# Kernel tuning notes

Hardware: AMD Instinct MI355X
Metric: run time of the kernel (lower is better)

The kernel has to match this reference:

```python
import jax, jax.numpy as jnp
import numpy as np

N, E, H, L = 50000, 400000, 100, 2
NF, EF = 16, 8
BN_EPS = 1e-5  # torch BatchNorm1d eps; eval mode with running_mean=0, running_var=1


def setup_inputs() -> dict:
    key = jax.random.key(0)
    ks = jax.random.split(key, 32)
    s = 0.05
    rn = lambda k, shape: jax.random.normal(k, shape, dtype=jnp.float32) * s
    return {
        "x": jax.random.normal(ks[0], (N, NF), dtype=jnp.float32),
        "edge_index": jax.random.randint(ks[1], (2, E), 0, N, dtype=jnp.int32),
        "edge_attr": jax.random.normal(ks[2], (E, EF), dtype=jnp.float32),
        "node_w": rn(ks[3], (NF, H)), "node_b": rn(ks[4], (H,)),
        "edge_w": rn(ks[5], (EF, H)), "edge_b": rn(ks[6], (H,)),
        "conv_w1": rn(ks[7], (L, H, H)), "conv_b1": rn(ks[8], (L, H)),
        "conv_w2": rn(ks[9], (L, H, H)), "conv_b2": rn(ks[10], (L, H)),
        "bn_gamma": jnp.ones((L, H), jnp.float32), "bn_beta": jnp.zeros((L, H), jnp.float32),
        "em_w1": rn(ks[11], (L, 3 * H, H)), "em_b1": rn(ks[12], (L, H)),
        "em_w2": rn(ks[13], (L, H, H)), "em_b2": rn(ks[14], (L, H)),
        "mlp_w1": rn(ks[15], (3 * H, 50)), "mlp_b1": rn(ks[16], (50,)),
        "mlp_w2": rn(ks[17], (50, 25)), "mlp_b2": rn(ks[18], (25,)),
        "mlp_w3": rn(ks[19], (25, 1)), "mlp_b3": rn(ks[20], (1,)),
    }


def reference(x, edge_index, edge_attr, node_w, node_b, edge_w, edge_b,
              conv_w1, conv_b1, conv_w2, conv_b2, bn_gamma, bn_beta,
              em_w1, em_b1, em_w2, em_b2,
              mlp_w1, mlp_b1, mlp_w2, mlp_b2, mlp_w3, mlp_b3):
    src, dst = edge_index[0], edge_index[1]
    h = x @ node_w + node_b            # [N,H]
    e = edge_attr @ edge_w + edge_b    # [E,H]
    bn_inv = 1.0 / jnp.sqrt(1.0 + BN_EPS)
    for i in range(L):
        # GINEConv (eps=0): MLP(x + sum_{j->i} relu(x_j + e_ji))
        msg = jax.nn.relu(h[src] + e)                                  # [E,H]
        agg = jax.ops.segment_sum(msg, dst, num_segments=h.shape[0])   # [N,H]
        z = h + agg
        z = jax.nn.relu(z @ conv_w1[i] + conv_b1[i]) @ conv_w2[i] + conv_b2[i]
        bn = z * (bn_gamma[i] * bn_inv) + bn_beta[i]                   # BN eval (mean 0, var 1)
        h = (h + jax.nn.relu(bn)) * 0.5
        ei = jnp.concatenate([h[src], h[dst], e], axis=-1)             # [E,3H]
        e = e + (jax.nn.relu(ei @ em_w1[i] + em_b1[i]) @ em_w2[i] + em_b2[i]) * 0.5
    xe = jnp.concatenate([h[src], h[dst], e], axis=-1)                 # [E,3H]
    o = jax.nn.relu(xe @ mlp_w1 + mlp_b1)
    o = jax.nn.relu(o @ mlp_w2 + mlp_b2)
    return (o @ mlp_w3 + mlp_b3)[:, 0]                                 # [E]
```

## Files before the change

### kernel.cpp

```cpp
#include <hip/hip_runtime.h>

#define HD 100
#define NF 16
#define EF 8
#define NN 50000
#define NE 400000
#define NT64 6250

typedef __attribute__((ext_vector_type(8))) short bf16x8;
typedef __attribute__((ext_vector_type(4))) float f32x4;

__device__ __forceinline__ float frelu(float v) { return v > 0.f ? v : 0.f; }
__device__ __forceinline__ unsigned short f2bf(float f) {
  unsigned int u = __float_as_uint(f);
  unsigned int r = (u + 0x7FFF + ((u >> 16) & 1)) >> 16;
  return (unsigned short)r;
}
__device__ __forceinline__ int SWZ(int row, int byte) { return byte ^ ((row & 7) << 4); }
__device__ __forceinline__ float4 L4(const float* p) { return *(const float4*)p; }
__device__ __forceinline__ uint2 pk4(float4 f) {
  uint2 o;
  o.x = (unsigned)f2bf(f.x) | ((unsigned)f2bf(f.y) << 16);
  o.y = (unsigned)f2bf(f.z) | ((unsigned)f2bf(f.w) << 16);
  return o;
}

__device__ __forceinline__ void pack_one(const float* __restrict__ W,
    unsigned short* __restrict__ out, int K, int N, int NT, int t) {
  int lane = t & 63, nt = (t >> 6) % NT, ks = (t >> 6) / NT;
  int kb = ks * 32 + (lane >> 4) * 8, n = nt * 16 + (lane & 15);
  unsigned short v[8];
  #pragma unroll
  for (int j = 0; j < 8; ++j) {
    int k = kb + j;
    float f = (k < K && n < N) ? W[(size_t)k * N + n] : 0.f;
    v[j] = f2bf(f);
  }
  uint4 o4;
  o4.x = (unsigned)v[0] | ((unsigned)v[1] << 16);
  o4.y = (unsigned)v[2] | ((unsigned)v[3] << 16);
  o4.z = (unsigned)v[4] | ((unsigned)v[5] << 16);
  o4.w = (unsigned)v[6] | ((unsigned)v[7] << 16);
  *(uint4*)&out[(size_t)t * 8] = o4;
}

__global__ __launch_bounds__(256) void k_pack_all(
    const float* __restrict__ em_w1, const float* __restrict__ em_w2,
    const float* __restrict__ mlp_w1,
    unsigned short* __restrict__ w1p0, unsigned short* __restrict__ w1p1,
    unsigned short* __restrict__ w2p0, unsigned short* __restrict__ w2p1,
    unsigned short* __restrict__ wf1p) {
  int t = blockIdx.x * 256 + threadIdx.x;
  if (t < 4480)        pack_one(em_w1,          w1p0, 300, 100, 7, t);
  else if (t < 8960)   pack_one(em_w1 + 30000,  w1p1, 300, 100, 7, t - 4480);
  else if (t < 10752)  pack_one(em_w2,          w2p0, 100, 100, 7, t - 8960);
  else if (t < 12544)  pack_one(em_w2 + 10000,  w2p1, 100, 100, 7, t - 10752);
  else if (t < 15104)  pack_one(mlp_w1,         wf1p, 300, 50, 4, t - 12544);
}

__global__ __launch_bounds__(256) void k_node_embed(const float* __restrict__ x,
    const float* __restrict__ w, const float* __restrict__ b, float* __restrict__ h) {
  int t = blockIdx.x * 256 + threadIdx.x;
  int n = t / HD, o = t % HD;
  if (n >= NN) return;
  float acc = b[o];
  #pragma unroll
  for (int k = 0; k < NF; ++k) acc = fmaf(x[n * NF + k], w[k * HD + o], acc);
  h[(size_t)n * HD + o] = acc;
}

__global__ __launch_bounds__(256) void k_edge_embed_perm(const float* __restrict__ ea,
    const int* __restrict__ eids, const float* __restrict__ w, const float* __restrict__ b,
    float* __restrict__ e) {
  __shared__ float ws_[EF * HD];
  __shared__ float bs_[HD];
  int tid = threadIdx.x;
  for (int i = tid; i < EF * HD; i += 256) ws_[i] = w[i];
  for (int i = tid; i < HD; i += 256) bs_[i] = b[i];
  __syncthreads();
  long long t = (long long)blockIdx.x * 256 + tid;
  int p = (int)(t / 25), c4 = (int)(t % 25);
  if (p >= NE) return;
  int eid = eids[p];
  const float* ap = ea + (size_t)eid * EF;
  float4 a0 = L4(ap), a1 = L4(ap + 4);
  float av[8] = {a0.x, a0.y, a0.z, a0.w, a1.x, a1.y, a1.z, a1.w};
  int c0 = c4 * 4;
  float o0 = bs_[c0], o1 = bs_[c0 + 1], o2 = bs_[c0 + 2], o3 = bs_[c0 + 3];
  #pragma unroll
  for (int k = 0; k < EF; ++k) {
    const float* wr = &ws_[k * HD + c0];
    o0 = fmaf(av[k], wr[0], o0); o1 = fmaf(av[k], wr[1], o1);
    o2 = fmaf(av[k], wr[2], o2); o3 = fmaf(av[k], wr[3], o3);
  }
  float4 o; o.x = o0; o.y = o1; o.z = o2; o.w = o3;
  ((float4*)e)[(size_t)p * 25 + c4] = o;
}

__global__ __launch_bounds__(256) void k_hist(const int* __restrict__ dst, int* __restrict__ deg) {
  int eid = blockIdx.x * 256 + threadIdx.x;
  if (eid < NE) atomicAdd(&deg[dst[eid]], 1);
}
__global__ __launch_bounds__(256) void k_scan_part(const int* __restrict__ deg, int* __restrict__ part) {
  __shared__ int sm[256];
  int i = blockIdx.x * 256 + threadIdx.x;
  sm[threadIdx.x] = (i < NN) ? deg[i] : 0;
  __syncthreads();
  for (int s = 128; s > 0; s >>= 1) {
    if (threadIdx.x < s) sm[threadIdx.x] += sm[threadIdx.x + s];
    __syncthreads();
  }
  if (threadIdx.x == 0) part[blockIdx.x] = sm[0];
}
__global__ __launch_bounds__(256) void k_scan_top(int* __restrict__ part, int nb) {
  __shared__ int sm[256];
  int v = (threadIdx.x < nb) ? part[threadIdx.x] : 0;
  sm[threadIdx.x] = v;
  __syncthreads();
  for (int off = 1; off < 256; off <<= 1) {
    int t = (threadIdx.x >= (unsigned)off) ? sm[threadIdx.x - off] : 0;
    __syncthreads();
    sm[threadIdx.x] += t;
    __syncthreads();
  }
  if (threadIdx.x < nb) part[threadIdx.x] = sm[threadIdx.x] - v;
}
__global__ __launch_bounds__(256) void k_scan_fill(const int* __restrict__ deg,
    const int* __restrict__ part, int* __restrict__ rowptr, int* __restrict__ cursor) {
  __shared__ int sm[256];
  int i = blockIdx.x * 256 + threadIdx.x;
  int v = (i < NN) ? deg[i] : 0;
  sm[threadIdx.x] = v;
  __syncthreads();
  for (int off = 1; off < 256; off <<= 1) {
    int t = (threadIdx.x >= (unsigned)off) ? sm[threadIdx.x - off] : 0;
    __syncthreads();
    sm[threadIdx.x] += t;
    __syncthreads();
  }
  int pfx = part[blockIdx.x] + sm[threadIdx.x] - v;
  if (i <= NN) rowptr[i] = pfx;
  if (i < NN) cursor[i] = pfx;
}
__global__ __launch_bounds__(256) void k_fill(const int* __restrict__ dst,
    int* __restrict__ cursor, int* __restrict__ eids) {
  int eid = blockIdx.x * 256 + threadIdx.x;
  if (eid >= NE) return;
  int pos = atomicAdd(&cursor[dst[eid]], 1);
  eids[pos] = eid;
}

__global__ __launch_bounds__(256) void k_gather_node(
    float* __restrict__ h, const float* __restrict__ e,
    const int* __restrict__ rowptr, const int* __restrict__ eids,
    const int* __restrict__ src,
    const float* __restrict__ w1, const float* __restrict__ b1,
    const float* __restrict__ w2, const float* __restrict__ b2,
    const float* __restrict__ gamma, const float* __restrict__ beta) {
  __shared__ float zs[64 * 101];
  int tid = threadIdx.x;
  int base = blockIdx.x * 64;
  {
    int slot = tid >> 2, sub = tid & 3;
    int n = base + slot;
    int cn = n < NN ? n : NN - 1;
    int r0 = rowptr[cn], r1 = rowptr[cn + 1];
    float4 acc[7];
    #pragma unroll
    for (int i = 0; i < 7; ++i) { acc[i].x = 0.f; acc[i].y = 0.f; acc[i].z = 0.f; acc[i].w = 0.f; }
    for (int p = r0; p < r1; ++p) {
      int s = src[eids[p]];
      const float4* hp = (const float4*)&h[(size_t)s * HD];
      const float4* ep = (const float4*)&e[(size_t)p * HD];
      #pragma unroll
      for (int i = 0; i < 7; ++i) {
        int c = sub + i * 4;
        if (c < 25) {
          float4 hv = hp[c], ev = ep[c];
          acc[i].x += frelu(hv.x + ev.x);
          acc[i].y += frelu(hv.y + ev.y);
          acc[i].z += frelu(hv.z + ev.z);
          acc[i].w += frelu(hv.w + ev.w);
        }
      }
    }
    const float4* hn = (const float4*)&h[(size_t)cn * HD];
    #pragma unroll
    for (int i = 0; i < 7; ++i) {
      int c = sub + i * 4;
      if (c < 25) {
        float4 hv = hn[c];
        float* zp = &zs[slot * 101 + c * 4];
        zp[0] = hv.x + acc[i].x;
        zp[1] = hv.y + acc[i].y;
        zp[2] = hv.z + acc[i].z;
        zp[3] = hv.w + acc[i].w;
      }
    }
  }
  __syncthreads();
  int el = tid & 63;
  int o0 = __builtin_amdgcn_readfirstlane((tid >> 6) * 25);
  float* row = &zs[el * 101];
  float acc[25];
  #pragma unroll
  for (int j = 0; j < 25; ++j) acc[j] = b1[o0 + j];
  for (int k = 0; k < HD; ++k) {
    float a = row[k];
    const float* wr = &w1[k * HD + o0];
    #pragma unroll
    for (int j = 0; j < 25; ++j) acc[j] = fmaf(a, wr[j], acc[j]);
  }
  __syncthreads();
  #pragma unroll
  for (int j = 0; j < 25; ++j) row[o0 + j] = frelu(acc[j]);
  __syncthreads();
  float acc2[25];
  #pragma unroll
  for (int j = 0; j < 25; ++j) acc2[j] = b2[o0 + j];
  for (int k = 0; k < HD; ++k) {
    float a = row[k];
    const float* wr = &w2[k * HD + o0];
    #pragma unroll
    for (int j = 0; j < 25; ++j) acc2[j] = fmaf(a, wr[j], acc2[j]);
  }
  int gn = base + el;
  if (gn < NN) {
    const float bninv = 0.99999500003749973f;
    #pragma unroll
    for (int j = 0; j < 25; ++j) {
      int o = o0 + j;
      float bn = acc2[j] * (gamma[o] * bninv) + beta[o];
      h[(size_t)gn * HD + o] = (h[(size_t)gn * HD + o] + frelu(bn)) * 0.5f;
    }
  }
}

__global__ __launch_bounds__(512) void k_edge_mfma(
    const float* __restrict__ h, float* __restrict__ e,
    const int* __restrict__ eids, const int* __restrict__ src, const int* __restrict__ dst,
    const unsigned short* __restrict__ w1p, const float* __restrict__ b1,
    const unsigned short* __restrict__ w2p, const float* __restrict__ b2) {
  __shared__ __align__(16) char lds[151040];
  char* W1L = lds;
  char* W2L = lds + 64512;
  char* A1  = lds + 93184;
  char* A2  = lds + 134144;
  int* ss  = (int*)(lds + 150528);
  int* ds_ = (int*)(lds + 150784);
  int tid = threadIdx.x;
  for (int i = tid; i < 4032; i += 512) ((uint4*)W1L)[i] = ((const uint4*)w1p)[i];
  for (int i = tid; i < 1792; i += 512) ((uint4*)W2L)[i] = ((const uint4*)w2p)[i];

  int lane = tid & 63, w = tid >> 6;
  int l15 = lane & 15, lq = lane >> 4;
  int g = w >> 2;
  int arow = (w & 3) * 16 + l15;
  int ntb = g * 4, ntc = g ? 3 : 4;
  f32x4 zero = {0.f, 0.f, 0.f, 0.f};

  for (int tile = blockIdx.x; tile < NT64; tile += gridDim.x) {
    int base = tile * 64;
    if (tid < 64) { int eid = eids[base + tid]; ss[tid] = src[eid]; ds_[tid] = dst[eid]; }
    __syncthreads();
    for (int idx = tid; idx < 64 * 25; idx += 512) {
      int row = idx / 25, c4 = idx % 25;
      float4 f = ((const float4*)e)[(size_t)(base + row) * 25 + c4];
      *(uint2*)(A1 + SWZ(row, row * 640 + 400 + c4 * 8)) = pk4(f);
    }
    for (int idx = tid; idx < 64 * 25; idx += 512) {
      int row = idx / 25, c4 = idx % 25;
      float4 f = ((const float4*)h)[(size_t)ss[row] * 25 + c4];
      *(uint2*)(A1 + SWZ(row, row * 640 + c4 * 8)) = pk4(f);
    }
    for (int idx = tid; idx < 64 * 25; idx += 512) {
      int row = idx / 25, c4 = idx % 25;
      float4 f = ((const float4*)h)[(size_t)ds_[row] * 25 + c4];
      *(uint2*)(A1 + SWZ(row, row * 640 + 200 + c4 * 8)) = pk4(f);
    }
    for (int idx = tid; idx < 64 * 5; idx += 512) {
      int row = idx / 5, j = idx % 5;
      uint2 z; z.x = 0u; z.y = 0u;
      *(uint2*)(A1 + SWZ(row, row * 640 + 600 + j * 8)) = z;
    }
    __syncthreads();
    f32x4 acc[4];
    #pragma unroll
    for (int i = 0; i < 4; ++i) acc[i] = zero;
    #pragma unroll
    for (int ks = 0; ks < 10; ++ks) {
      bf16x8 a = *(const bf16x8*)(A1 + SWZ(arow, arow * 640 + (ks * 32 + lq * 8) * 2));
      #pragma unroll
      for (int i = 0; i < 4; ++i) {
        if (i < ntc) {
          int nt = ntb + i;
          bf16x8 b = (ks < 9)
            ? *(const bf16x8*)(W1L + ks * 7168 + (nt * 64 + lane) * 16)
            : *(const bf16x8*)(w1p + (size_t)9 * 3584 + (nt * 64 + lane) * 8);
          acc[i] = __builtin_amdgcn_mfma_f32_16x16x32_bf16(a, b, acc[i], 0, 0, 0);
        }
      }
    }
    #pragma unroll
    for (int i = 0; i < 4; ++i) {
      if (i < ntc) {
        int o = (ntb + i) * 16 + l15;
        float bias = (o < HD) ? b1[o] : 0.f;
        #pragma unroll
        for (int ii = 0; ii < 4; ++ii) {
          int r = (w & 3) * 16 + lq * 4 + ii;
          float v = acc[i][ii] + bias;
          v = (o < HD) ? frelu(v) : 0.f;
          *(unsigned short*)(A2 + SWZ(r, r * 256 + o * 2)) = f2bf(v);
        }
      }
    }
    for (int idx = tid; idx < 64 * 8; idx += 512) {
      int r = idx / 8, c = idx % 8;
      *(unsigned int*)(A2 + SWZ(r, r * 256 + 224 + c * 4)) = 0;
    }
    __syncthreads();
    f32x4 acc2[4];
    #pragma unroll
    for (int i = 0; i < 4; ++i) acc2[i] = zero;
    #pragma unroll
    for (int ks = 0; ks < 4; ++ks) {
      bf16x8 a = *(const bf16x8*)(A2 + SWZ(arow, arow * 256 + (ks * 32 + lq * 8) * 2));
      #pragma unroll
      for (int i = 0; i < 4; ++i) {
        if (i < ntc) {
          int nt = ntb + i;
          bf16x8 b = *(const bf16x8*)(W2L + ks * 7168 + (nt * 64 + lane) * 16);
          acc2[i] = __builtin_amdgcn_mfma_f32_16x16x32_bf16(a, b, acc2[i], 0, 0, 0);
        }
      }
    }
    #pragma unroll
    for (int i = 0; i < 4; ++i) {
      if (i < ntc) {
        int o = (ntb + i) * 16 + l15;
        if (o < HD) {
          float bias = b2[o];
          #pragma unroll
          for (int ii = 0; ii < 4; ++ii) {
            int r = (w & 3) * 16 + lq * 4 + ii;
            size_t pp = (size_t)(base + r) * HD + o;
            e[pp] = e[pp] + 0.5f * (acc2[i][ii] + bias);
          }
        }
      }
    }
    __syncthreads();
  }
}

__global__ __launch_bounds__(512) void k_edge_final_mfma(
    const float* __restrict__ h, const float* __restrict__ e,
    const int* __restrict__ eids, const int* __restrict__ src, const int* __restrict__ dst,
    const unsigned short* __restrict__ w1p, const float* __restrict__ b1,
    const unsigned short* __restrict__ w2p, const float* __restrict__ b2,
    const unsigned short* __restrict__ wf1p, const float* __restrict__ fb1,
    const float* __restrict__ fw2, const float* __restrict__ fb2,
    const float* __restrict__ fw3, const float* __restrict__ fb3,
    float* __restrict__ out) {
  __shared__ __align__(16) char lds[156500];
  char* W1L = lds;
  char* W2L = lds + 64512;
  char* A1  = lds + 93184;
  char* A2  = lds + 134144;
  float* W2s = (float*)(lds + 150528);
  float* b2s = (float*)(lds + 155528);
  float* W3s = (float*)(lds + 155628);
  float* b3s = (float*)(lds + 155728);
  int* es  = (int*)(lds + 155732);
  int* ss  = (int*)(lds + 155988);
  int* ds_ = (int*)(lds + 156244);
  int tid = threadIdx.x;
  for (int i = tid; i < 4032; i += 512) ((uint4*)W1L)[i] = ((const uint4*)w1p)[i];
  for (int i = tid; i < 1792; i += 512) ((uint4*)W2L)[i] = ((const uint4*)w2p)[i];
  for (int i = tid; i < 1250; i += 512) W2s[i] = fw2[i];
  if (tid < 25) { b2s[tid] = fb2[tid]; W3s[tid] = fw3[tid]; }
  if (tid == 0) b3s[0] = fb3[0];

  int lane = tid & 63, w = tid >> 6;
  int l15 = lane & 15, lq = lane >> 4;
  int g = w >> 2;
  int arow = (w & 3) * 16 + l15;
  int ntb = g * 4, ntc = g ? 3 : 4;
  f32x4 zero = {0.f, 0.f, 0.f, 0.f};

  for (int tile = blockIdx.x; tile < NT64; tile += gridDim.x) {
    int base = tile * 64;
    if (tid < 64) {
      int eid = eids[base + tid];
      es[tid] = eid; ss[tid] = src[eid]; ds_[tid] = dst[eid];
    }
    __syncthreads();
    for (int idx = tid; idx < 64 * 25; idx += 512) {
      int row = idx / 25, c4 = idx % 25;
      float4 f = ((const float4*)e)[(size_t)(base + row) * 25 + c4];
      *(uint2*)(A1 + SWZ(row, row * 640 + 400 + c4 * 8)) = pk4(f);
    }
    for (int idx = tid; idx < 64 * 25; idx += 512) {
      int row = idx / 25, c4 = idx % 25;
      float4 f = ((const float4*)h)[(size_t)ss[row] * 25 + c4];
      *(uint2*)(A1 + SWZ(row, row * 640 + c4 * 8)) = pk4(f);
    }
    for (int idx = tid; idx < 64 * 25; idx += 512) {
      int row = idx / 25, c4 = idx % 25;
      float4 f = ((const float4*)h)[(size_t)ds_[row] * 25 + c4];
      *(uint2*)(A1 + SWZ(row, row * 640 + 200 + c4 * 8)) = pk4(f);
    }
    for (int idx = tid; idx < 64 * 5; idx += 512) {
      int row = idx / 5, j = idx % 5;
      uint2 z; z.x = 0u; z.y = 0u;
      *(uint2*)(A1 + SWZ(row, row * 640 + 600 + j * 8)) = z;
    }
    __syncthreads();
    f32x4 acc[4];
    #pragma unroll
    for (int i = 0; i < 4; ++i) acc[i] = zero;
    #pragma unroll
    for (int ks = 0; ks < 10; ++ks) {
      bf16x8 a = *(const bf16x8*)(A1 + SWZ(arow, arow * 640 + (ks * 32 + lq * 8) * 2));
      #pragma unroll
      for (int i = 0; i < 4; ++i) {
        if (i < ntc) {
          int nt = ntb + i;
          bf16x8 b = (ks < 9)
            ? *(const bf16x8*)(W1L + ks * 7168 + (nt * 64 + lane) * 16)
            : *(const bf16x8*)(w1p + (size_t)9 * 3584 + (nt * 64 + lane) * 8);
          acc[i] = __builtin_amdgcn_mfma_f32_16x16x32_bf16(a, b, acc[i], 0, 0, 0);
        }
      }
    }
    #pragma unroll
    for (int i = 0; i < 4; ++i) {
      if (i < ntc) {
        int o = (ntb + i) * 16 + l15;
        float bias = (o < HD) ? b1[o] : 0.f;
        #pragma unroll
        for (int ii = 0; ii < 4; ++ii) {
          int r = (w & 3) * 16 + lq * 4 + ii;
          float v = acc[i][ii] + bias;
          v = (o < HD) ? frelu(v) : 0.f;
          *(unsigned short*)(A2 + SWZ(r, r * 256 + o * 2)) = f2bf(v);
        }
      }
    }
    for (int idx = tid; idx < 64 * 8; idx += 512) {
      int r = idx / 8, c = idx % 8;
      *(unsigned int*)(A2 + SWZ(r, r * 256 + 224 + c * 4)) = 0;
    }
    __syncthreads();
    f32x4 acc2[4];
    #pragma unroll
    for (int i = 0; i < 4; ++i) acc2[i] = zero;
    #pragma unroll
    for (int ks = 0; ks < 4; ++ks) {
      bf16x8 a = *(const bf16x8*)(A2 + SWZ(arow, arow * 256 + (ks * 32 + lq * 8) * 2));
      #pragma unroll
      for (int i = 0; i < 4; ++i) {
        if (i < ntc) {
          int nt = ntb + i;
          bf16x8 b = *(const bf16x8*)(W2L + ks * 7168 + (nt * 64 + lane) * 16);
          acc2[i] = __builtin_amdgcn_mfma_f32_16x16x32_bf16(a, b, acc2[i], 0, 0, 0);
        }
      }
    }
    #pragma unroll
    for (int i = 0; i < 4; ++i) {
      if (i < ntc) {
        int o = (ntb + i) * 16 + l15;
        if (o < HD) {
          float bias = b2[o];
          #pragma unroll
          for (int ii = 0; ii < 4; ++ii) {
            int r = (w & 3) * 16 + lq * 4 + ii;
            float ne = e[(size_t)(base + r) * HD + o] + 0.5f * (acc2[i][ii] + bias);
            *(unsigned short*)(A1 + SWZ(r, r * 640 + (200 + o) * 2)) = f2bf(ne);
          }
        }
      }
    }
    __syncthreads();
    f32x4 acc3[2];
    acc3[0] = zero; acc3[1] = zero;
    #pragma unroll
    for (int ks = 0; ks < 10; ++ks) {
      bf16x8 a = *(const bf16x8*)(A1 + SWZ(arow, arow * 640 + (ks * 32 + lq * 8) * 2));
      #pragma unroll
      for (int i = 0; i < 2; ++i) {
        int nt = g * 2 + i;
        bf16x8 b = *(const bf16x8*)(wf1p + ((size_t)(ks * 4 + nt) * 64 + lane) * 8);
        acc3[i] = __builtin_amdgcn_mfma_f32_16x16x32_bf16(a, b, acc3[i], 0, 0, 0);
      }
    }
    __syncthreads();
    #pragma unroll
    for (int i = 0; i < 2; ++i) {
      int o = (g * 2 + i) * 16 + l15;
      if (o < 50) {
        float bias = fb1[o];
        #pragma unroll
        for (int ii = 0; ii < 4; ++ii) {
          int r = (w & 3) * 16 + lq * 4 + ii;
          *(float*)(A2 + r * 208 + o * 4) = frelu(acc3[i][ii] + bias);
        }
      }
    }
    __syncthreads();
    {
      int elg = tid >> 3, q8 = tid & 7;
      const float* trow = (const float*)(A2 + elg * 208);
      float s[4];
      {
        int i = 0;
        #pragma unroll
        for (int j0 = 0; j0 < 25; j0 += 8) { if (j0 + q8 < 25) s[i++] = b2s[j0 + q8]; }
      }
      for (int k = 0; k < 50; ++k) {
        float tv = trow[k];
        int i = 0;
        #pragma unroll
        for (int j0 = 0; j0 < 25; j0 += 8) {
          if (j0 + q8 < 25) { s[i] = fmaf(tv, W2s[k * 25 + j0 + q8], s[i]); ++i; }
        }
      }
      float racc = 0.f;
      {
        int i = 0;
        #pragma unroll
        for (int j0 = 0; j0 < 25; j0 += 8) {
          if (j0 + q8 < 25) { racc = fmaf(frelu(s[i]), W3s[j0 + q8], racc); ++i; }
        }
      }
      racc += __shfl_xor(racc, 1, 8);
      racc += __shfl_xor(racc, 2, 8);
      racc += __shfl_xor(racc, 4, 8);
      if (q8 == 0) out[es[elg]] = racc + b3s[0];
    }
    __syncthreads();
  }
}

extern "C" void kernel_launch(void* const* d_in, const int* in_sizes, int n_in,
                              void* d_out, int out_size, void* d_ws, size_t ws_size,
                              hipStream_t stream) {
  (void)in_sizes; (void)n_in; (void)out_size; (void)ws_size;
  const float* x       = (const float*)d_in[0];
  const int*   eidx    = (const int*)  d_in[1];
  const float* eattr   = (const float*)d_in[2];
  const float* node_w  = (const float*)d_in[3];
  const float* node_b  = (const float*)d_in[4];
  const float* edge_w  = (const float*)d_in[5];
  const float* edge_b  = (const float*)d_in[6];
  const float* conv_w1 = (const float*)d_in[7];
  const float* conv_b1 = (const float*)d_in[8];
  const float* conv_w2 = (const float*)d_in[9];
  const float* conv_b2 = (const float*)d_in[10];
  const float* bn_g    = (const float*)d_in[11];
  const float* bn_b    = (const float*)d_in[12];
  const float* em_w1   = (const float*)d_in[13];
  const float* em_b1   = (const float*)d_in[14];
  const float* em_w2   = (const float*)d_in[15];
  const float* em_b2   = (const float*)d_in[16];
  const float* mlp_w1  = (const float*)d_in[17];
  const float* mlp_b1  = (const float*)d_in[18];
  const float* mlp_w2  = (const float*)d_in[19];
  const float* mlp_b2  = (const float*)d_in[20];
  const float* mlp_w3  = (const float*)d_in[21];
  const float* mlp_b3  = (const float*)d_in[22];

  const int* src = eidx;
  const int* dst = eidx + NE;

  char* ws = (char*)d_ws;
  float* h    = (float*)(ws);
  float* e    = (float*)(ws + 40000000);
  unsigned short* w1p0 = (unsigned short*)(ws + 200000000);
  unsigned short* w1p1 = (unsigned short*)(ws + 200071680);
  unsigned short* w2p0 = (unsigned short*)(ws + 200143360);
  unsigned short* w2p1 = (unsigned short*)(ws + 200172032);
  unsigned short* wf1p = (unsigned short*)(ws + 200200704);
  int* rowptr = (int*)(ws + 200241664);
  int* cursor = (int*)(ws + 200442112);
  int* eids   = (int*)(ws + 200642112);
  int* part   = (int*)(ws + 202242112);

  const int SCAN_NB = (NN + 256) / 256;
  hipMemsetAsync(cursor, 0, (size_t)NN * 4, stream);
  k_hist<<<(NE + 255) / 256, 256, 0, stream>>>(dst, cursor);
  k_scan_part<<<SCAN_NB, 256, 0, stream>>>(cursor, part);
  k_scan_top<<<1, 256, 0, stream>>>(part, SCAN_NB);
  k_scan_fill<<<SCAN_NB, 256, 0, stream>>>(cursor, part, rowptr, cursor);
  k_fill<<<(NE + 255) / 256, 256, 0, stream>>>(dst, cursor, eids);

  k_pack_all<<<(15104 + 255) / 256, 256, 0, stream>>>(
      em_w1, em_w2, mlp_w1, w1p0, w1p1, w2p0, w2p1, wf1p);

  k_node_embed<<<(NN * HD + 255) / 256, 256, 0, stream>>>(x, node_w, node_b, h);
  {
    long long th = (long long)NE * 25;
    k_edge_embed_perm<<<(unsigned)((th + 255) / 256), 256, 0, stream>>>(eattr, eids, edge_w, edge_b, e);
  }

  for (int i = 0; i < 2; ++i) {
    k_gather_node<<<(NN + 63) / 64, 256, 0, stream>>>(
        h, e, rowptr, eids, src,
        conv_w1 + i * HD * HD, conv_b1 + i * HD,
        conv_w2 + i * HD * HD, conv_b2 + i * HD, bn_g + i * HD, bn_b + i * HD);
    if (i == 0) {
      k_edge_mfma<<<256, 512, 0, stream>>>(
          h, e, eids, src, dst, w1p0, em_b1, w2p0, em_b2);
    } else {
      k_edge_final_mfma<<<256, 512, 0, stream>>>(
          h, e, eids, src, dst, w1p1, em_b1 + HD, w2p1, em_b2 + HD,
          wf1p, mlp_b1, mlp_w2, mlp_b2, mlp_w3, mlp_b3, (float*)d_out);
    }
  }
}
```

Before: 835.6 us.

## Double edge-MLP block size to 1024 threads and split N-tiles across more waves

The two edge-MLP MFMA kernels now launch 16 waves per block instead of 8. Each wave group owns two output N-tiles instead of four, and in the final kernel one tile for the first MLP layer. The extra waves are meant to hide LDS and gather latency, since LDS use (about 150 KB) already limits each CU to one block. The tail scalar MLP stage runs on only half the threads, and the larger block may raise register pressure under the 1024-thread launch bound.

```diff
diff --git a/kernel.cpp b/kernel.cpp
--- a/kernel.cpp
+++ b/kernel.cpp
@@ -236,7 +236,7 @@
   }
 }
 
-__global__ __launch_bounds__(512) void k_edge_mfma(
+__global__ __launch_bounds__(1024) void k_edge_mfma(
     const float* __restrict__ h, float* __restrict__ e,
     const int* __restrict__ eids, const int* __restrict__ src, const int* __restrict__ dst,
     const unsigned short* __restrict__ w1p, const float* __restrict__ b1,
@@ -249,49 +249,48 @@
   int* ss  = (int*)(lds + 150528);
   int* ds_ = (int*)(lds + 150784);
   int tid = threadIdx.x;
-  for (int i = tid; i < 4032; i += 512) ((uint4*)W1L)[i] = ((const uint4*)w1p)[i];
-  for (int i = tid; i < 1792; i += 512) ((uint4*)W2L)[i] = ((const uint4*)w2p)[i];
+  for (int i = tid; i < 4032; i += 1024) ((uint4*)W1L)[i] = ((const uint4*)w1p)[i];
+  for (int i = tid; i < 1792; i += 1024) ((uint4*)W2L)[i] = ((const uint4*)w2p)[i];
 
   int lane = tid & 63, w = tid >> 6;
   int l15 = lane & 15, lq = lane >> 4;
   int g = w >> 2;
   int arow = (w & 3) * 16 + l15;
-  int ntb = g * 4, ntc = g ? 3 : 4;
+  int ntb = g * 2, ntc = (g == 3) ? 1 : 2;
   f32x4 zero = {0.f, 0.f, 0.f, 0.f};
 
   for (int tile = blockIdx.x; tile < NT64; tile += gridDim.x) {
     int base = tile * 64;
     if (tid < 64) { int eid = eids[base + tid]; ss[tid] = src[eid]; ds_[tid] = dst[eid]; }
     __syncthreads();
-    for (int idx = tid; idx < 64 * 25; idx += 512) {
+    for (int idx = tid; idx < 64 * 25; idx += 1024) {
       int row = idx / 25, c4 = idx % 25;
       float4 f = ((const float4*)e)[(size_t)(base + row) * 25 + c4];
       *(uint2*)(A1 + SWZ(row, row * 640 + 400 + c4 * 8)) = pk4(f);
     }
-    for (int idx = tid; idx < 64 * 25; idx += 512) {
+    for (int idx = tid; idx < 64 * 25; idx += 1024) {
       int row = idx / 25, c4 = idx % 25;
       float4 f = ((const float4*)h)[(size_t)ss[row] * 25 + c4];
       *(uint2*)(A1 + SWZ(row, row * 640 + c4 * 8)) = pk4(f);
     }
-    for (int idx = tid; idx < 64 * 25; idx += 512) {
+    for (int idx = tid; idx < 64 * 25; idx += 1024) {
       int row = idx / 25, c4 = idx % 25;
       float4 f = ((const float4*)h)[(size_t)ds_[row] * 25 + c4];
       *(uint2*)(A1 + SWZ(row, row * 640 + 200 + c4 * 8)) = pk4(f);
     }
-    for (int idx = tid; idx < 64 * 5; idx += 512) {
-      int row = idx / 5, j = idx % 5;
+    if (tid < 320) {
+      int row = tid / 5, j = tid % 5;
       uint2 z; z.x = 0u; z.y = 0u;
       *(uint2*)(A1 + SWZ(row, row * 640 + 600 + j * 8)) = z;
     }
     __syncthreads();
-    f32x4 acc[4];
-    #pragma unroll
-    for (int i = 0; i < 4; ++i) acc[i] = zero;
+    f32x4 acc[2];
+    acc[0] = zero; acc[1] = zero;
     #pragma unroll
     for (int ks = 0; ks < 10; ++ks) {
       bf16x8 a = *(const bf16x8*)(A1 + SWZ(arow, arow * 640 + (ks * 32 + lq * 8) * 2));
       #pragma unroll
-      for (int i = 0; i < 4; ++i) {
+      for (int i = 0; i < 2; ++i) {
         if (i < ntc) {
           int nt = ntb + i;
           bf16x8 b = (ks < 9)
@@ -302,7 +301,7 @@
       }
     }
     #pragma unroll
-    for (int i = 0; i < 4; ++i) {
+    for (int i = 0; i < 2; ++i) {
       if (i < ntc) {
         int o = (ntb + i) * 16 + l15;
         float bias = (o < HD) ? b1[o] : 0.f;
@@ -315,19 +314,18 @@
         }
       }
     }
-    for (int idx = tid; idx < 64 * 8; idx += 512) {
-      int r = idx / 8, c = idx % 8;
+    if (tid < 512) {
+      int r = tid / 8, c = tid % 8;
       *(unsigned int*)(A2 + SWZ(r, r * 256 + 224 + c * 4)) = 0;
     }
     __syncthreads();
-    f32x4 acc2[4];
-    #pragma unroll
-    for (int i = 0; i < 4; ++i) acc2[i] = zero;
+    f32x4 acc2[2];
+    acc2[0] = zero; acc2[1] = zero;
     #pragma unroll
     for (int ks = 0; ks < 4; ++ks) {
       bf16x8 a = *(const bf16x8*)(A2 + SWZ(arow, arow * 256 + (ks * 32 + lq * 8) * 2));
       #pragma unroll
-      for (int i = 0; i < 4; ++i) {
+      for (int i = 0; i < 2; ++i) {
         if (i < ntc) {
           int nt = ntb + i;
           bf16x8 b = *(const bf16x8*)(W2L + ks * 7168 + (nt * 64 + lane) * 16);
@@ -336,7 +334,7 @@
       }
     }
     #pragma unroll
-    for (int i = 0; i < 4; ++i) {
+    for (int i = 0; i < 2; ++i) {
       if (i < ntc) {
         int o = (ntb + i) * 16 + l15;
         if (o < HD) {
@@ -354,7 +352,7 @@
   }
 }
 
-__global__ __launch_bounds__(512) void k_edge_final_mfma(
+__global__ __launch_bounds__(1024) void k_edge_final_mfma(
     const float* __restrict__ h, const float* __restrict__ e,
     const int* __restrict__ eids, const int* __restrict__ src, const int* __restrict__ dst,
     const unsigned short* __restrict__ w1p, const float* __restrict__ b1,
@@ -376,9 +374,9 @@
   int* ss  = (int*)(lds + 155988);
   int* ds_ = (int*)(lds + 156244);
   int tid = threadIdx.x;
-  for (int i = tid; i < 4032; i += 512) ((uint4*)W1L)[i] = ((const uint4*)w1p)[i];
-  for (int i = tid; i < 1792; i += 512) ((uint4*)W2L)[i] = ((const uint4*)w2p)[i];
-  for (int i = tid; i < 1250; i += 512) W2s[i] = fw2[i];
+  for (int i = tid; i < 4032; i += 1024) ((uint4*)W1L)[i] = ((const uint4*)w1p)[i];
+  for (int i = tid; i < 1792; i += 1024) ((uint4*)W2L)[i] = ((const uint4*)w2p)[i];
+  for (int i = tid; i < 1250; i += 1024) W2s[i] = fw2[i];
   if (tid < 25) { b2s[tid] = fb2[tid]; W3s[tid] = fw3[tid]; }
   if (tid == 0) b3s[0] = fb3[0];
 
@@ -386,7 +384,7 @@
   int l15 = lane & 15, lq = lane >> 4;
   int g = w >> 2;
   int arow = (w & 3) * 16 + l15;
-  int ntb = g * 4, ntc = g ? 3 : 4;
+  int ntb = g * 2, ntc = (g == 3) ? 1 : 2;
   f32x4 zero = {0.f, 0.f, 0.f, 0.f};
 
   for (int tile = blockIdx.x; tile < NT64; tile += gridDim.x) {
@@ -396,35 +394,34 @@
       es[tid] = eid; ss[tid] = src[eid]; ds_[tid] = dst[eid];
     }
     __syncthreads();
-    for (int idx = tid; idx < 64 * 25; idx += 512) {
+    for (int idx = tid; idx < 64 * 25; idx += 1024) {
       int row = idx / 25, c4 = idx % 25;
       float4 f = ((const float4*)e)[(size_t)(base + row) * 25 + c4];
       *(uint2*)(A1 + SWZ(row, row * 640 + 400 + c4 * 8)) = pk4(f);
     }
-    for (int idx = tid; idx < 64 * 25; idx += 512) {
+    for (int idx = tid; idx < 64 * 25; idx += 1024) {
       int row = idx / 25, c4 = idx % 25;
       float4 f = ((const float4*)h)[(size_t)ss[row] * 25 + c4];
       *(uint2*)(A1 + SWZ(row, row * 640 + c4 * 8)) = pk4(f);
     }
-    for (int idx = tid; idx < 64 * 25; idx += 512) {
+    for (int idx = tid; idx < 64 * 25; idx += 1024) {
       int row = idx / 25, c4 = idx % 25;
       float4 f = ((const float4*)h)[(size_t)ds_[row] * 25 + c4];
       *(uint2*)(A1 + SWZ(row, row * 640 + 200 + c4 * 8)) = pk4(f);
     }
-    for (int idx = tid; idx < 64 * 5; idx += 512) {
-      int row = idx / 5, j = idx % 5;
+    if (tid < 320) {
+      int row = tid / 5, j = tid % 5;
       uint2 z; z.x = 0u; z.y = 0u;
       *(uint2*)(A1 + SWZ(row, row * 640 + 600 + j * 8)) = z;
     }
     __syncthreads();
-    f32x4 acc[4];
-    #pragma unroll
-    for (int i = 0; i < 4; ++i) acc[i] = zero;
+    f32x4 acc[2];
+    acc[0] = zero; acc[1] = zero;
     #pragma unroll
     for (int ks = 0; ks < 10; ++ks) {
       bf16x8 a = *(const bf16x8*)(A1 + SWZ(arow, arow * 640 + (ks * 32 + lq * 8) * 2));
       #pragma unroll
-      for (int i = 0; i < 4; ++i) {
+      for (int i = 0; i < 2; ++i) {
         if (i < ntc) {
           int nt = ntb + i;
           bf16x8 b = (ks < 9)
@@ -435,7 +432,7 @@
       }
     }
     #pragma unroll
-    for (int i = 0; i < 4; ++i) {
+    for (int i = 0; i < 2; ++i) {
       if (i < ntc) {
         int o = (ntb + i) * 16 + l15;
         float bias = (o < HD) ? b1[o] : 0.f;
@@ -448,19 +445,18 @@
         }
       }
     }
-    for (int idx = tid; idx < 64 * 8; idx += 512) {
-      int r = idx / 8, c = idx % 8;
+    if (tid < 512) {
+      int r = tid / 8, c = tid % 8;
       *(unsigned int*)(A2 + SWZ(r, r * 256 + 224 + c * 4)) = 0;
     }
     __syncthreads();
-    f32x4 acc2[4];
-    #pragma unroll
-    for (int i = 0; i < 4; ++i) acc2[i] = zero;
+    f32x4 acc2[2];
+    acc2[0] = zero; acc2[1] = zero;
     #pragma unroll
     for (int ks = 0; ks < 4; ++ks) {
       bf16x8 a = *(const bf16x8*)(A2 + SWZ(arow, arow * 256 + (ks * 32 + lq * 8) * 2));
       #pragma unroll
-      for (int i = 0; i < 4; ++i) {
+      for (int i = 0; i < 2; ++i) {
         if (i < ntc) {
           int nt = ntb + i;
           bf16x8 b = *(const bf16x8*)(W2L + ks * 7168 + (nt * 64 + lane) * 16);
@@ -469,7 +465,7 @@
       }
     }
     #pragma unroll
-    for (int i = 0; i < 4; ++i) {
+    for (int i = 0; i < 2; ++i) {
       if (i < ntc) {
         int o = (ntb + i) * 16 + l15;
         if (o < HD) {
@@ -484,33 +480,27 @@
       }
     }
     __syncthreads();
-    f32x4 acc3[2];
-    acc3[0] = zero; acc3[1] = zero;
+    f32x4 acc3 = zero;
     #pragma unroll
     for (int ks = 0; ks < 10; ++ks) {
       bf16x8 a = *(const bf16x8*)(A1 + SWZ(arow, arow * 640 + (ks * 32 + lq * 8) * 2));
-      #pragma unroll
-      for (int i = 0; i < 2; ++i) {
-        int nt = g * 2 + i;
-        bf16x8 b = *(const bf16x8*)(wf1p + ((size_t)(ks * 4 + nt) * 64 + lane) * 8);
-        acc3[i] = __builtin_amdgcn_mfma_f32_16x16x32_bf16(a, b, acc3[i], 0, 0, 0);
-      }
-    }
-    __syncthreads();
-    #pragma unroll
-    for (int i = 0; i < 2; ++i) {
-      int o = (g * 2 + i) * 16 + l15;
+      bf16x8 b = *(const bf16x8*)(wf1p + ((size_t)(ks * 4 + g) * 64 + lane) * 8);
+      acc3 = __builtin_amdgcn_mfma_f32_16x16x32_bf16(a, b, acc3, 0, 0, 0);
+    }
+    __syncthreads();
+    {
+      int o = g * 16 + l15;
       if (o < 50) {
         float bias = fb1[o];
         #pragma unroll
         for (int ii = 0; ii < 4; ++ii) {
           int r = (w & 3) * 16 + lq * 4 + ii;
-          *(float*)(A2 + r * 208 + o * 4) = frelu(acc3[i][ii] + bias);
-        }
-      }
-    }
-    __syncthreads();
-    {
+          *(float*)(A2 + r * 208 + o * 4) = frelu(acc3[ii] + bias);
+        }
+      }
+    }
+    __syncthreads();
+    if (tid < 512) {
       int elg = tid >> 3, q8 = tid & 7;
       const float* trow = (const float*)(A2 + elg * 208);
       float s[4];
@@ -611,10 +601,10 @@
         conv_w1 + i * HD * HD, conv_b1 + i * HD,
         conv_w2 + i * HD * HD, conv_b2 + i * HD, bn_g + i * HD, bn_b + i * HD);
     if (i == 0) {
-      k_edge_mfma<<<256, 512, 0, stream>>>(
+      k_edge_mfma<<<256, 1024, 0, stream>>>(
           h, e, eids, src, dst, w1p0, em_b1, w2p0, em_b2);
     } else {
-      k_edge_final_mfma<<<256, 512, 0, stream>>>(
+      k_edge_final_mfma<<<256, 1024, 0, stream>>>(
           h, e, eids, src, dst, w1p1, em_b1 + HD, w2p1, em_b2 + HD,
           wf1p, mlp_b1, mlp_w2, mlp_b2, mlp_w3, mlp_b3, (float*)d_out);
     }
```

Measured after the change: 757.3 us. -9.4%, faster.
